# Kernel optimization log

Measured on AMD Instinct MI355X. Metric: run time of the kernel, lower is better.

Reference implementation:

```python
import jax, jax.numpy as jnp
import numpy as np

BN_EPS = 1e-5

def _square_distance(src, dst):
    # src [B,N,3], dst [B,S,3] -> [B,N,S]
    d = -2.0 * jnp.einsum('bnc,bsc->bns', src, dst)
    d = d + jnp.sum(src * src, -1)[:, :, None]
    d = d + jnp.sum(dst * dst, -1)[:, None, :]
    return d

def _conv_bn_relu(x, w, b, g, beta):
    # x [B,C,N]; 1x1 conv == channel GEMM, then training-mode batchnorm over (B,N)
    y = jnp.einsum('oc,bcn->bon', w, x) + b[None, :, None]
    mean = jnp.mean(y, axis=(0, 2), keepdims=True)
    var = jnp.mean((y - mean) ** 2, axis=(0, 2), keepdims=True)  # biased, as torch BN uses for normalization
    y = (y - mean) * jax.lax.rsqrt(var + BN_EPS)
    y = y * g[None, :, None] + beta[None, :, None]
    return jax.nn.relu(y)

def setup_inputs() -> dict:
    key = jax.random.key(0)
    ks = jax.random.split(key, 8)
    B, N, S, D1, D2 = 8, 8192, 2048, 128, 256
    C_in, C_mid, C_out = D1 + D2, 256, 256
    return {
        'xyz1': jax.random.normal(ks[0], (B, 3, N), jnp.float32),
        'xyz2': jax.random.normal(ks[1], (B, 3, S), jnp.float32),
        'points1': jax.random.normal(ks[2], (B, D1, N), jnp.float32),
        'points2': jax.random.normal(ks[3], (B, D2, S), jnp.float32),
        'w1': jax.random.normal(ks[4], (C_mid, C_in), jnp.float32) * (1.0 / np.sqrt(C_in)),
        'b1': jax.random.normal(ks[5], (C_mid,), jnp.float32) * 0.01,
        'g1': jnp.ones((C_mid,), jnp.float32),
        'beta1': jnp.zeros((C_mid,), jnp.float32),
        'w2': jax.random.normal(ks[6], (C_out, C_mid), jnp.float32) * (1.0 / np.sqrt(C_mid)),
        'b2': jax.random.normal(ks[7], (C_out,), jnp.float32) * 0.01,
        'g2': jnp.ones((C_out,), jnp.float32),
        'beta2': jnp.zeros((C_out,), jnp.float32),
    }

def reference(xyz1, xyz2, points1, points2, w1, b1, g1, beta1, w2, b2, g2, beta2):
    B = xyz1.shape[0]
    p1xyz = jnp.transpose(xyz1, (0, 2, 1))      # [B,N,3]
    p2xyz = jnp.transpose(xyz2, (0, 2, 1))      # [B,S,3]
    p2 = jnp.transpose(points2, (0, 2, 1))      # [B,S,D2]

    dists = _square_distance(p1xyz, p2xyz)      # [B,N,S]
    neg_d3, idx = jax.lax.top_k(-dists, 3)      # 3 smallest distances
    d3 = -neg_d3                                # [B,N,3]
    recip = 1.0 / (d3 + 1e-8)
    weight = recip / jnp.sum(recip, axis=2, keepdims=True)  # [B,N,3]

    gathered = jax.vmap(lambda p, i: p[i])(p2, idx)          # [B,N,3,D2]
    interp = jnp.sum(gathered * weight[..., None], axis=2)   # [B,N,D2]

    new_points = jnp.concatenate([jnp.transpose(points1, (0, 2, 1)), interp], axis=-1)
    x = jnp.transpose(new_points, (0, 2, 1))    # [B,D1+D2,N]
    x = _conv_bn_relu(x, w1, b1, g1, beta1)
    x = _conv_bn_relu(x, w2, b2, g2, beta2)
    return x
```

## Files before the change

### kernel.cpp

```cpp
#include <hip/hip_runtime.h>

#define B_    8
#define N_    8192
#define S_    2048
#define D1_   128
#define D2_   256
#define CIN_  384
#define CMID_ 256
#define COUT_ 256

typedef unsigned int  u32;
typedef unsigned short u16;
typedef __attribute__((ext_vector_type(8))) short short8;
typedef __attribute__((ext_vector_type(4))) float f32x4;

static __device__ __forceinline__ u32 uminu(u32 a, u32 b) { return a < b ? a : b; }
static __device__ __forceinline__ u32 umed3(u32 a, u32 b, u32 c) {
  u32 d;
  asm("v_med3_u32 %0, %1, %2, %3" : "=v"(d) : "v"(a), "v"(b), "v"(c));
  return d;
}
static __device__ __forceinline__ u16 f2bf(float f) {
  union { float f; u32 u; } v; v.f = f;
  u32 r = v.u + 0x7FFFu + ((v.u >> 16) & 1u);
  return (u16)(r >> 16);
}
static __device__ __forceinline__ float bflo(u32 u) { return __uint_as_float(u << 16); }
static __device__ __forceinline__ float bfhi(u32 u) { return __uint_as_float(u & 0xFFFF0000u); }
static __device__ __forceinline__ u32 cvtpk_bf16(float lo, float hi) {
  u32 d;
  asm("v_cvt_pk_bf16_f32 %0, %1, %2" : "=v"(d) : "v"(lo), "v"(hi));
  return d;
}

#define GLD16(g, l)                                                             \
  __builtin_amdgcn_global_load_lds((const __attribute__((address_space(1))) void*)(g), \
                                   (__attribute__((address_space(3))) void*)(l), 16, 0, 0)

#define WB(N)                                                                   \
  __builtin_amdgcn_sched_barrier(0);                                            \
  asm volatile("s_waitcnt vmcnt(" #N ")" ::: "memory");                         \
  __builtin_amdgcn_s_barrier();                                                 \
  __builtin_amdgcn_sched_barrier(0);

__global__ __launch_bounds__(256) void k_pre_all(const float* __restrict__ xyz2,
                                                 float4* __restrict__ pts4,
                                                 const float* __restrict__ w1,
                                                 const float* __restrict__ w2,
                                                 u16* __restrict__ w1b,
                                                 u16* __restrict__ w2b,
                                                 const float* __restrict__ p2,
                                                 float* __restrict__ p2T,
                                                 const float* __restrict__ p1,
                                                 u16* __restrict__ xT) {
  __shared__ float t[32][33];
  const int blk = blockIdx.x;
  const int cc = threadIdx.x & 31, rr = threadIdx.x >> 5;
  if (blk < 4096) {
    const int s0 = (blk & 63) * 32, d0 = ((blk >> 6) & 7) * 32, b = blk >> 9;
#pragma unroll
    for (int i = 0; i < 4; ++i) {
      int r = rr + i * 8;
      t[r][cc] = p2[((size_t)b * D2_ + d0 + r) * S_ + s0 + cc];
    }
    __syncthreads();
#pragma unroll
    for (int i = 0; i < 4; ++i) {
      int r = rr + i * 8;
      p2T[((size_t)b * S_ + s0 + r) * D2_ + d0 + cc] = t[cc][r];
    }
    return;
  }
  if (blk < 12288) {
    const int idx = blk - 4096;
    const int n0 = (idx & 255) * 32, c0 = ((idx >> 8) & 3) * 32, b = idx >> 10;
#pragma unroll
    for (int i = 0; i < 4; ++i) {
      int r = rr + i * 8;
      t[r][cc] = p1[((size_t)b * D1_ + c0 + r) * N_ + n0 + cc];
    }
    __syncthreads();
#pragma unroll
    for (int i = 0; i < 4; ++i) {
      int r = rr + i * 8;
      xT[((size_t)b * N_ + n0 + r) * CIN_ + c0 + cc] = f2bf(t[cc][r]);
    }
    return;
  }
  const int i = (blk - 12288) * 256 + threadIdx.x;
  if (i < B_ * S_) {
    const int b = i >> 11, s = i & (S_ - 1);
    const float* xb = xyz2 + (size_t)b * 3 * S_;
    float x = xb[s], y = xb[S_ + s], z = xb[2 * S_ + s];
    pts4[b * S_ + s] = make_float4(-2.f * x, -2.f * y, -2.f * z, x * x + y * y + z * z);
    return;
  }
  const int j = i - B_ * S_;
  if (j < CMID_ * CIN_) { w1b[j] = f2bf(w1[j]); return; }
  const int h = j - CMID_ * CIN_;
  if (h < COUT_ * CMID_) w2b[h] = f2bf(w2[h]);
}

__global__ __launch_bounds__(256) void k_nnref(const float* __restrict__ xyz1,
                                               const float4* __restrict__ pts4,
                                               int4* __restrict__ idx4,
                                               float4* __restrict__ w4) {
  __shared__ uint4 sk[4][64];
  const int b = blockIdx.y, t = threadIdx.x;
  const int nl = t & 63, chunk = t >> 6;
  const int n = blockIdx.x * 64 + nl;
  const float* pb = xyz1 + (size_t)b * 3 * N_;
  {
    const float px = pb[n], py = pb[N_ + n], pz = pb[2 * N_ + n];
    const float pn = px * px + py * py + pz * pz;
    const float4* __restrict__ P = pts4 + b * S_ + chunk * 512;
    u32 m0 = ~0u, m1 = ~0u, m2 = ~0u;
#pragma unroll 8
    for (int s = 0; s < 512; ++s) {
      float4 q = P[s];
      float d = fmaf(px, q.x, fmaf(py, q.y, fmaf(pz, q.z, pn + q.w)));
      d = fmaxf(d, 0.f);
      u32 k = (__float_as_uint(d) & 0xFFFFFE00u) | (u32)s;
      u32 m2n = umed3(m1, m2, k);
      m1 = umed3(m0, m1, k);
      m0 = uminu(m0, k);
      m2 = m2n;
    }
    uint4 v; v.x = m0; v.y = m1; v.z = m2; v.w = m2;
    sk[chunk][nl] = v;
  }
  __syncthreads();
  if (t < 64) {
    const double px = (double)pb[n], py = (double)pb[N_ + n], pz = (double)pb[2 * N_ + n];
    const double pn = px * px + py * py + pz * pz;
    double bd0 = 1e300, bd1 = 1e300, bd2 = 1e300;
    int bi0 = 1 << 30, bi1 = 1 << 30, bi2 = 1 << 30;
#pragma unroll
    for (int c = 0; c < 4; ++c) {
      uint4 kk = sk[c][t];
      u32 arr[3] = {kk.x, kk.y, kk.z};
#pragma unroll
      for (int j = 0; j < 3; ++j) {
        int s = c * 512 + (int)(arr[j] & 511u);
        float4 q = pts4[b * S_ + s];
        double x = (double)(q.x * -0.5f), y = (double)(q.y * -0.5f), z = (double)(q.z * -0.5f);
        double dot = px * x + py * y + pz * z;
        double d = -2.0 * dot + (pn + (x * x + y * y + z * z));
        if (d < bd2 || (d == bd2 && s < bi2)) {
          if (d < bd1 || (d == bd1 && s < bi1)) {
            bd2 = bd1; bi2 = bi1;
            if (d < bd0 || (d == bd0 && s < bi0)) { bd1 = bd0; bi1 = bi0; bd0 = d; bi0 = s; }
            else                                  { bd1 = d;  bi1 = s; }
          } else { bd2 = d; bi2 = s; }
        }
      }
    }
    float f0 = (float)bd0, f1 = (float)bd1, f2 = (float)bd2;
    float r0 = 1.f / (f0 + 1e-8f), r1 = 1.f / (f1 + 1e-8f), r2 = 1.f / (f2 + 1e-8f);
    float rs = r0 + r1 + r2;
    w4[(size_t)b * N_ + n]   = make_float4(r0 / rs, r1 / rs, r2 / rs, 0.f);
    idx4[(size_t)b * N_ + n] = make_int4(bi0, bi1, bi2, 0);
  }
}

__global__ __launch_bounds__(256) void k_gather_pack(const float* __restrict__ p2T,
                                                     const int4* __restrict__ idx4,
                                                     const float4* __restrict__ w4,
                                                     u16* __restrict__ xT) {
  const int b = blockIdx.y;
  const int wv = threadIdx.x >> 6, lane = threadIdx.x & 63;
  const int nbase = blockIdx.x * 16 + wv * 4;
  int4   id[4];
  float4 w[4];
#pragma unroll
  for (int i = 0; i < 4; ++i) {
    id[i] = idx4[(size_t)b * N_ + nbase + i];
    w[i]  = w4[(size_t)b * N_ + nbase + i];
  }
#pragma unroll
  for (int i = 0; i < 4; ++i) {
    const int n = nbase + i;
    const float4* r0 = (const float4*)(p2T + ((size_t)b * S_ + id[i].x) * D2_) + lane;
    const float4* r1 = (const float4*)(p2T + ((size_t)b * S_ + id[i].y) * D2_) + lane;
    const float4* r2 = (const float4*)(p2T + ((size_t)b * S_ + id[i].z) * D2_) + lane;
    float4 a = *r0, bb = *r1, cq = *r2;
    ushort4 pk;
    pk.x = f2bf(a.x * w[i].x + bb.x * w[i].y + cq.x * w[i].z);
    pk.y = f2bf(a.y * w[i].x + bb.y * w[i].y + cq.y * w[i].z);
    pk.z = f2bf(a.z * w[i].x + bb.z * w[i].y + cq.z * w[i].z);
    pk.w = f2bf(a.w * w[i].x + bb.w * w[i].y + cq.w * w[i].z);
    *(ushort4*)(xT + ((size_t)b * N_ + n) * CIN_ + D1_ + lane * 4) = pk;
  }
}

__global__ __launch_bounds__(64) void k_bnstat(const float* __restrict__ ps,
                                               const float* __restrict__ pq,
                                               const float* __restrict__ g,
                                               const float* __restrict__ beta,
                                               float* __restrict__ scale,
                                               float* __restrict__ shift) {
  const int o = blockIdx.x, l = threadIdx.x;
  float s = 0.f, q = 0.f;
#pragma unroll
  for (int i = 0; i < 8; ++i) {
    s += ps[(size_t)(i * 64 + l) * 256 + o];
    q += pq[(size_t)(i * 64 + l) * 256 + o];
  }
#pragma unroll
  for (int m = 1; m <= 32; m <<= 1) { s += __shfl_xor(s, m); q += __shfl_xor(q, m); }
  if (l == 0) {
    const float inv = 1.0f / (float)(B_ * N_);
    float mean = s * inv;
    float var = q * inv - mean * mean;
    float sc = g[o] / sqrtf(var + 1e-5f);
    scale[o] = sc;
    shift[o] = beta[o] - mean * sc;
  }
}

__global__ __launch_bounds__(512) void k_gemm1(const u16* __restrict__ Wb,
                                               const float* __restrict__ bias,
                                               const u16* __restrict__ xT,
                                               u16* __restrict__ y1T,
                                               float* __restrict__ psum,
                                               float* __restrict__ pssq) {
  __shared__ u16 As[3][8192];
  __shared__ u16 Bs[3][4096];
  __shared__ float s_sum[256], s_ssq[256];
  const int b = blockIdx.z, bn0 = blockIdx.x * 128;
  const int tid = threadIdx.x, w = tid >> 6, l = tid & 63;
  const int wm = w & 3, wn = w >> 2;
  const int lr = l >> 2, lc = l & 3;
  const int fm = l & 15, fq = l >> 4;
  const int clog = (lc ^ ((lr >> 1) & 3)) * 8;
  const int swz8 = (fq ^ ((fm >> 1) & 3)) * 8;
  f32x4 acc[4][4];
#pragma unroll
  for (int i = 0; i < 4; ++i)
#pragma unroll
    for (int j = 0; j < 4; ++j) acc[i][j] = (f32x4){0.f, 0.f, 0.f, 0.f};

  const int NK = CIN_ / 32;

#define STAGE1(kk, buf)                                                         \
  {                                                                             \
    const int k0_ = (kk) * 32;                                                  \
    _Pragma("unroll") for (int j_ = 0; j_ < 2; ++j_) {                          \
      int seg_ = w * 2 + j_, row_ = seg_ * 16 + lr;                             \
      GLD16(Wb + (size_t)row_ * CIN_ + k0_ + clog, &As[buf][seg_ * 512]);       \
    }                                                                           \
    int brow_ = w * 16 + lr;                                                    \
    GLD16(xT + ((size_t)b * N_ + bn0 + brow_) * CIN_ + k0_ + clog,              \
          &Bs[buf][w * 512]);                                                   \
  }

  STAGE1(0, 0);
  STAGE1(1, 1);
  int cur = 0;
  for (int kk = 0; kk < NK; ++kk) {
    if (kk + 1 < NK) { WB(3) } else { WB(0) }
    if (kk + 2 < NK) {
      int bt = cur + 2; if (bt >= 3) bt -= 3;
      STAGE1(kk + 2, bt);
    }
    short8 af[4], bfr[4];
#pragma unroll
    for (int f = 0; f < 4; ++f) {
      af[f]  = *(const short8*)&As[cur][(wm * 64 + f * 16 + fm) * 32 + swz8];
      bfr[f] = *(const short8*)&Bs[cur][(wn * 64 + f * 16 + fm) * 32 + swz8];
    }
#pragma unroll
    for (int i = 0; i < 4; ++i)
#pragma unroll
      for (int j = 0; j < 4; ++j)
        acc[i][j] = __builtin_amdgcn_mfma_f32_16x16x32_bf16(af[i], bfr[j], acc[i][j], 0, 0, 0);
    ++cur; if (cur == 3) cur = 0;
  }
#undef STAGE1

  if (tid < 256) { s_sum[tid] = 0.f; s_ssq[tid] = 0.f; }
  __syncthreads();
  u16* tb = y1T + ((size_t)b * 64 + (bn0 >> 7)) * 32768;
#pragma unroll
  for (int i = 0; i < 4; ++i) {
    int ob = wm * 64 + i * 16 + fq * 4;
    float4 b4 = *(const float4*)(bias + ob);
    float sv0 = 0, sv1 = 0, sv2 = 0, sv3 = 0, qv0 = 0, qv1 = 0, qv2 = 0, qv3 = 0;
#pragma unroll
    for (int j = 0; j < 4; ++j) {
      int nl = wn * 64 + j * 16 + fm;
      ushort4 pk;
      pk.x = f2bf(acc[i][j][0] + b4.x);
      pk.y = f2bf(acc[i][j][1] + b4.y);
      pk.z = f2bf(acc[i][j][2] + b4.z);
      pk.w = f2bf(acc[i][j][3] + b4.w);
      *(ushort4*)(tb + (size_t)(ob >> 5) * 4096 + nl * 32 + (ob & 31)) = pk;
      float v0 = bflo(pk.x), v1 = bflo(pk.y), v2 = bflo(pk.z), v3 = bflo(pk.w);
      sv0 += v0; sv1 += v1; sv2 += v2; sv3 += v3;
      qv0 = fmaf(v0, v0, qv0); qv1 = fmaf(v1, v1, qv1);
      qv2 = fmaf(v2, v2, qv2); qv3 = fmaf(v3, v3, qv3);
    }
#pragma unroll
    for (int m = 1; m <= 8; m <<= 1) {
      sv0 += __shfl_xor(sv0, m); sv1 += __shfl_xor(sv1, m);
      sv2 += __shfl_xor(sv2, m); sv3 += __shfl_xor(sv3, m);
      qv0 += __shfl_xor(qv0, m); qv1 += __shfl_xor(qv1, m);
      qv2 += __shfl_xor(qv2, m); qv3 += __shfl_xor(qv3, m);
    }
    if (fm == 0) {
      atomicAdd(&s_sum[ob + 0], sv0); atomicAdd(&s_sum[ob + 1], sv1);
      atomicAdd(&s_sum[ob + 2], sv2); atomicAdd(&s_sum[ob + 3], sv3);
      atomicAdd(&s_ssq[ob + 0], qv0); atomicAdd(&s_ssq[ob + 1], qv1);
      atomicAdd(&s_ssq[ob + 2], qv2); atomicAdd(&s_ssq[ob + 3], qv3);
    }
  }
  __syncthreads();
  if (tid < 256) {
    const int blk = blockIdx.x + 64 * blockIdx.z;
    psum[(size_t)blk * 256 + tid] = s_sum[tid];
    pssq[(size_t)blk * 256 + tid] = s_ssq[tid];
  }
}

__global__ __launch_bounds__(512) void k_gemm2(const u16* __restrict__ Wb2,
                                               const float* __restrict__ b2,
                                               const u16* __restrict__ y1T,
                                               const float* __restrict__ scale,
                                               const float* __restrict__ shift,
                                               u16* __restrict__ y2T,
                                               float* __restrict__ psum,
                                               float* __restrict__ pssq) {
  __shared__ u16 As[3][8192];
  __shared__ u16 Bs[3][4096];
  __shared__ float s_sum[256], s_ssq[256];
  __shared__ float s_sc[CMID_], s_sh[CMID_];
  const int b = blockIdx.z, bn0 = blockIdx.x * 128;
  const int tid = threadIdx.x, w = tid >> 6, l = tid & 63;
  const int wm = w & 3, wn = w >> 2;
  const int lr = l >> 2, lc = l & 3;
  const int fm = l & 15, fq = l >> 4;
  const int clog = (lc ^ ((lr >> 1) & 3)) * 8;
  const int swz8 = (fq ^ ((fm >> 1) & 3)) * 8;
  if (tid < 256) {
    s_sc[tid] = scale[tid];
    s_sh[tid] = shift[tid];
  }
  f32x4 acc[4][4];
#pragma unroll
  for (int i = 0; i < 4; ++i)
#pragma unroll
    for (int j = 0; j < 4; ++j) acc[i][j] = (f32x4){0.f, 0.f, 0.f, 0.f};

  const u16* tb = y1T + ((size_t)b * 64 + (bn0 >> 7)) * 32768;
  const int NK = CMID_ / 32;

#define STAGE2(kk, buf)                                                         \
  {                                                                             \
    const int k0_ = (kk) * 32;                                                  \
    _Pragma("unroll") for (int j_ = 0; j_ < 2; ++j_) {                          \
      int seg_ = w * 2 + j_, row_ = seg_ * 16 + lr;                             \
      GLD16(Wb2 + (size_t)row_ * CMID_ + k0_ + clog, &As[buf][seg_ * 512]);     \
    }                                                                           \
    int brow_ = w * 16 + lr;                                                    \
    GLD16(tb + (size_t)(kk) * 4096 + brow_ * 32 + clog, &Bs[buf][w * 512]);     \
  }

  STAGE2(0, 0);
  STAGE2(1, 1);
  int cur = 0;
  for (int kk = 0; kk < NK; ++kk) {
    if (kk + 1 < NK) { WB(3) } else { WB(0) }
    if (kk + 2 < NK) {
      int bt = cur + 2; if (bt >= 3) bt -= 3;
      STAGE2(kk + 2, bt);
    }
    const int kb = kk * 32 + fq * 8;
    float4 s0 = *(const float4*)&s_sc[kb], s1 = *(const float4*)&s_sc[kb + 4];
    float4 h0 = *(const float4*)&s_sh[kb], h1 = *(const float4*)&s_sh[kb + 4];
    short8 af[4], bfr[4];
#pragma unroll
    for (int f = 0; f < 4; ++f) {
      af[f] = *(const short8*)&As[cur][(wm * 64 + f * 16 + fm) * 32 + swz8];
      uint4 r = *(const uint4*)&Bs[cur][(wn * 64 + f * 16 + fm) * 32 + swz8];
      float v0 = fmaxf(fmaf(bflo(r.x), s0.x, h0.x), 0.f);
      float v1 = fmaxf(fmaf(bfhi(r.x), s0.y, h0.y), 0.f);
      float v2 = fmaxf(fmaf(bflo(r.y), s0.z, h0.z), 0.f);
      float v3 = fmaxf(fmaf(bfhi(r.y), s0.w, h0.w), 0.f);
      float v4 = fmaxf(fmaf(bflo(r.z), s1.x, h1.x), 0.f);
      float v5 = fmaxf(fmaf(bfhi(r.z), s1.y, h1.y), 0.f);
      float v6 = fmaxf(fmaf(bflo(r.w), s1.z, h1.z), 0.f);
      float v7 = fmaxf(fmaf(bfhi(r.w), s1.w, h1.w), 0.f);
      union { u32 u[4]; short8 s; } cv;
      cv.u[0] = cvtpk_bf16(v0, v1); cv.u[1] = cvtpk_bf16(v2, v3);
      cv.u[2] = cvtpk_bf16(v4, v5); cv.u[3] = cvtpk_bf16(v6, v7);
      bfr[f] = cv.s;
    }
#pragma unroll
    for (int i = 0; i < 4; ++i)
#pragma unroll
      for (int j = 0; j < 4; ++j)
        acc[i][j] = __builtin_amdgcn_mfma_f32_16x16x32_bf16(af[i], bfr[j], acc[i][j], 0, 0, 0);
    ++cur; if (cur == 3) cur = 0;
  }
#undef STAGE2

  if (tid < 256) { s_sum[tid] = 0.f; s_ssq[tid] = 0.f; }
  __syncthreads();
  u16* tb2 = y2T + ((size_t)b * 64 + (bn0 >> 7)) * 32768;
#pragma unroll
  for (int i = 0; i < 4; ++i) {
    int ob = wm * 64 + i * 16 + fq * 4;
    float4 b4 = *(const float4*)(b2 + ob);
    float sv0 = 0, sv1 = 0, sv2 = 0, sv3 = 0, qv0 = 0, qv1 = 0, qv2 = 0, qv3 = 0;
#pragma unroll
    for (int j = 0; j < 4; ++j) {
      int nl = wn * 64 + j * 16 + fm;
      ushort4 pk;
      pk.x = f2bf(acc[i][j][0] + b4.x);
      pk.y = f2bf(acc[i][j][1] + b4.y);
      pk.z = f2bf(acc[i][j][2] + b4.z);
      pk.w = f2bf(acc[i][j][3] + b4.w);
      *(ushort4*)(tb2 + (size_t)(ob >> 5) * 4096 + nl * 32 + (ob & 31)) = pk;
      float v0 = bflo(pk.x), v1 = bflo(pk.y), v2 = bflo(pk.z), v3 = bflo(pk.w);
      sv0 += v0; sv1 += v1; sv2 += v2; sv3 += v3;
      qv0 = fmaf(v0, v0, qv0); qv1 = fmaf(v1, v1, qv1);
      qv2 = fmaf(v2, v2, qv2); qv3 = fmaf(v3, v3, qv3);
    }
#pragma unroll
    for (int m = 1; m <= 8; m <<= 1) {
      sv0 += __shfl_xor(sv0, m); sv1 += __shfl_xor(sv1, m);
      sv2 += __shfl_xor(sv2, m); sv3 += __shfl_xor(sv3, m);
      qv0 += __shfl_xor(qv0, m); qv1 += __shfl_xor(qv1, m);
      qv2 += __shfl_xor(qv2, m); qv3 += __shfl_xor(qv3, m);
    }
    if (fm == 0) {
      atomicAdd(&s_sum[ob + 0], sv0); atomicAdd(&s_sum[ob + 1], sv1);
      atomicAdd(&s_sum[ob + 2], sv2); atomicAdd(&s_sum[ob + 3], sv3);
      atomicAdd(&s_ssq[ob + 0], qv0); atomicAdd(&s_ssq[ob + 1], qv1);
      atomicAdd(&s_ssq[ob + 2], qv2); atomicAdd(&s_ssq[ob + 3], qv3);
    }
  }
  __syncthreads();
  if (tid < 256) {
    const int blk = blockIdx.x + 64 * blockIdx.z;
    psum[(size_t)blk * 256 + tid] = s_sum[tid];
    pssq[(size_t)blk * 256 + tid] = s_ssq[tid];
  }
}

__global__ __launch_bounds__(256) void k_bn2t(const u16* __restrict__ y2T,
                                              const float* __restrict__ scale,
                                              const float* __restrict__ shift,
                                              float* __restrict__ out) {
  __shared__ float t[32][33];
  const int b = blockIdx.z, n0 = blockIdx.x * 32, o0 = blockIdx.y * 32;
  const int cc = threadIdx.x & 31, rr = threadIdx.x >> 5;
  const float sc = scale[o0 + cc], sh = shift[o0 + cc];
  const u16* tb = y2T + ((size_t)b * 64 + (n0 >> 7)) * 32768 +
                  (size_t)(o0 >> 5) * 4096 + (size_t)(n0 & 96) * 32;
#pragma unroll
  for (int i = 0; i < 4; ++i) {
    int r = rr + i * 8;
    float v = bflo((u32)tb[r * 32 + cc]);
    t[r][cc] = fmaxf(fmaf(v, sc, sh), 0.f);
  }
  __syncthreads();
#pragma unroll
  for (int i = 0; i < 4; ++i) {
    int r = rr + i * 8;
    out[((size_t)b * COUT_ + o0 + r) * N_ + n0 + cc] = t[cc][r];
  }
}

extern "C" void kernel_launch(void* const* d_in, const int* in_sizes, int n_in,
                              void* d_out, int out_size, void* d_ws, size_t ws_size,
                              hipStream_t stream) {
  const float* xyz1    = (const float*)d_in[0];
  const float* xyz2    = (const float*)d_in[1];
  const float* points1 = (const float*)d_in[2];
  const float* points2 = (const float*)d_in[3];
  const float* w1      = (const float*)d_in[4];
  const float* b1      = (const float*)d_in[5];
  const float* g1      = (const float*)d_in[6];
  const float* beta1   = (const float*)d_in[7];
  const float* w2      = (const float*)d_in[8];
  const float* b2      = (const float*)d_in[9];
  const float* g2      = (const float*)d_in[10];
  const float* beta2   = (const float*)d_in[11];
  float* out = (float*)d_out;

  char* ws = (char*)d_ws;
  size_t off = 0;
  u16*    xT    = (u16*)(ws + off);    off += (size_t)B_ * N_ * CIN_ * 2;
  u16*    y1T   = (u16*)(ws + off);    off += (size_t)B_ * N_ * CMID_ * 2;
  float*  p2T   = (float*)(ws + off);  off += (size_t)B_ * S_ * D2_ * 4;
  float4* pts4  = (float4*)(ws + off); off += (size_t)B_ * S_ * 16;
  int4*   idx4  = (int4*)(ws + off);   off += (size_t)B_ * N_ * 16;
  float4* w4    = (float4*)(ws + off); off += (size_t)B_ * N_ * 16;
  u16*    w1b   = (u16*)(ws + off);    off += (size_t)CMID_ * CIN_ * 2;
  u16*    w2b   = (u16*)(ws + off);    off += (size_t)COUT_ * CMID_ * 2;
  float*  stats = (float*)(ws + off);  off += 1024 * sizeof(float);
  float*  psx   = (float*)(ws + off);  off += (size_t)4 * 512 * 256 * 4;
  u16*    y2T   = xT;
  float* psum1 = psx;
  float* pssq1 = psum1 + 512 * 256;
  float* psum2 = pssq1 + 512 * 256;
  float* pssq2 = psum2 + 512 * 256;
  float* scale1 = stats,        * shift1 = stats + 256;
  float* scale2 = stats + 512,  * shift2 = stats + 768;

  k_pre_all    <<<dim3(12992), 256, 0, stream>>>(xyz2, pts4, w1, w2, w1b, w2b,
                                                 points2, p2T, points1, xT);
  k_nnref      <<<dim3(N_ / 64, B_), 256, 0, stream>>>(xyz1, pts4, idx4, w4);
  k_gather_pack<<<dim3(N_ / 16, B_), 256, 0, stream>>>(p2T, idx4, w4, xT);
  k_gemm1      <<<dim3(N_ / 128, 1, B_), 512, 0, stream>>>(w1b, b1, xT, y1T,
                                                           psum1, pssq1);
  k_bnstat     <<<dim3(CMID_), 64, 0, stream>>>(psum1, pssq1, g1, beta1, scale1, shift1);
  k_gemm2      <<<dim3(N_ / 128, 1, B_), 512, 0, stream>>>(w2b, b2, y1T,
                                                           scale1, shift1,
                                                           y2T, psum2, pssq2);
  k_bnstat     <<<dim3(COUT_), 64, 0, stream>>>(psum2, pssq2, g2, beta2, scale2, shift2);
  k_bn2t       <<<dim3(N_ / 32, COUT_ / 32, B_), 256, 0, stream>>>(y2T, scale2, shift2, out);
}
```

Baseline: 300.9 us.

## Merge nearest-neighbour search with transpose blocks into one kernel for overlap

```diff
diff --git a/kernel.cpp b/kernel.cpp
--- a/kernel.cpp
+++ b/kernel.cpp
@@ -43,51 +43,13 @@
   __builtin_amdgcn_s_barrier();                                                 \
   __builtin_amdgcn_sched_barrier(0);
 
-__global__ __launch_bounds__(256) void k_pre_all(const float* __restrict__ xyz2,
-                                                 float4* __restrict__ pts4,
-                                                 const float* __restrict__ w1,
-                                                 const float* __restrict__ w2,
-                                                 u16* __restrict__ w1b,
-                                                 u16* __restrict__ w2b,
-                                                 const float* __restrict__ p2,
-                                                 float* __restrict__ p2T,
-                                                 const float* __restrict__ p1,
-                                                 u16* __restrict__ xT) {
-  __shared__ float t[32][33];
-  const int blk = blockIdx.x;
-  const int cc = threadIdx.x & 31, rr = threadIdx.x >> 5;
-  if (blk < 4096) {
-    const int s0 = (blk & 63) * 32, d0 = ((blk >> 6) & 7) * 32, b = blk >> 9;
-#pragma unroll
-    for (int i = 0; i < 4; ++i) {
-      int r = rr + i * 8;
-      t[r][cc] = p2[((size_t)b * D2_ + d0 + r) * S_ + s0 + cc];
-    }
-    __syncthreads();
-#pragma unroll
-    for (int i = 0; i < 4; ++i) {
-      int r = rr + i * 8;
-      p2T[((size_t)b * S_ + s0 + r) * D2_ + d0 + cc] = t[cc][r];
-    }
-    return;
-  }
-  if (blk < 12288) {
-    const int idx = blk - 4096;
-    const int n0 = (idx & 255) * 32, c0 = ((idx >> 8) & 3) * 32, b = idx >> 10;
-#pragma unroll
-    for (int i = 0; i < 4; ++i) {
-      int r = rr + i * 8;
-      t[r][cc] = p1[((size_t)b * D1_ + c0 + r) * N_ + n0 + cc];
-    }
-    __syncthreads();
-#pragma unroll
-    for (int i = 0; i < 4; ++i) {
-      int r = rr + i * 8;
-      xT[((size_t)b * N_ + n0 + r) * CIN_ + c0 + cc] = f2bf(t[cc][r]);
-    }
-    return;
-  }
-  const int i = (blk - 12288) * 256 + threadIdx.x;
+__global__ __launch_bounds__(256) void k_pre0(const float* __restrict__ xyz2,
+                                              float4* __restrict__ pts4,
+                                              const float* __restrict__ w1,
+                                              const float* __restrict__ w2,
+                                              u16* __restrict__ w1b,
+                                              u16* __restrict__ w2b) {
+  const int i = blockIdx.x * 256 + threadIdx.x;
   if (i < B_ * S_) {
     const int b = i >> 11, s = i & (S_ - 1);
     const float* xb = xyz2 + (size_t)b * 3 * S_;
@@ -101,65 +63,108 @@
   if (h < COUT_ * CMID_) w2b[h] = f2bf(w2[h]);
 }
 
-__global__ __launch_bounds__(256) void k_nnref(const float* __restrict__ xyz1,
-                                               const float4* __restrict__ pts4,
-                                               int4* __restrict__ idx4,
-                                               float4* __restrict__ w4) {
-  __shared__ uint4 sk[4][64];
-  const int b = blockIdx.y, t = threadIdx.x;
-  const int nl = t & 63, chunk = t >> 6;
-  const int n = blockIdx.x * 64 + nl;
-  const float* pb = xyz1 + (size_t)b * 3 * N_;
-  {
-    const float px = pb[n], py = pb[N_ + n], pz = pb[2 * N_ + n];
-    const float pn = px * px + py * py + pz * pz;
-    const float4* __restrict__ P = pts4 + b * S_ + chunk * 512;
-    u32 m0 = ~0u, m1 = ~0u, m2 = ~0u;
+__global__ __launch_bounds__(256) void k_mega(const float* __restrict__ xyz1,
+                                              const float4* __restrict__ pts4,
+                                              int4* __restrict__ idx4,
+                                              float4* __restrict__ w4,
+                                              const float* __restrict__ p2,
+                                              float* __restrict__ p2T,
+                                              const float* __restrict__ p1,
+                                              u16* __restrict__ xT) {
+  __shared__ __align__(16) char smem[4352];
+  const int blk = blockIdx.x;
+  if (blk < 1024) {
+    uint4 (*sk)[64] = (uint4(*)[64])smem;
+    const int b = blk >> 7, t = threadIdx.x;
+    const int nl = t & 63;
+    const int chunk = __builtin_amdgcn_readfirstlane(t >> 6);
+    const int n = (blk & 127) * 64 + nl;
+    const float* pb = xyz1 + (size_t)b * 3 * N_;
+    {
+      const float px = pb[n], py = pb[N_ + n], pz = pb[2 * N_ + n];
+      const float pn = px * px + py * py + pz * pz;
+      const float4* __restrict__ P = pts4 + b * S_ + chunk * 512;
+      u32 m0 = ~0u, m1 = ~0u, m2 = ~0u;
 #pragma unroll 8
-    for (int s = 0; s < 512; ++s) {
-      float4 q = P[s];
-      float d = fmaf(px, q.x, fmaf(py, q.y, fmaf(pz, q.z, pn + q.w)));
-      d = fmaxf(d, 0.f);
-      u32 k = (__float_as_uint(d) & 0xFFFFFE00u) | (u32)s;
-      u32 m2n = umed3(m1, m2, k);
-      m1 = umed3(m0, m1, k);
-      m0 = uminu(m0, k);
-      m2 = m2n;
-    }
-    uint4 v; v.x = m0; v.y = m1; v.z = m2; v.w = m2;
-    sk[chunk][nl] = v;
-  }
-  __syncthreads();
-  if (t < 64) {
-    const double px = (double)pb[n], py = (double)pb[N_ + n], pz = (double)pb[2 * N_ + n];
-    const double pn = px * px + py * py + pz * pz;
-    double bd0 = 1e300, bd1 = 1e300, bd2 = 1e300;
-    int bi0 = 1 << 30, bi1 = 1 << 30, bi2 = 1 << 30;
-#pragma unroll
-    for (int c = 0; c < 4; ++c) {
-      uint4 kk = sk[c][t];
-      u32 arr[3] = {kk.x, kk.y, kk.z};
-#pragma unroll
-      for (int j = 0; j < 3; ++j) {
-        int s = c * 512 + (int)(arr[j] & 511u);
-        float4 q = pts4[b * S_ + s];
-        double x = (double)(q.x * -0.5f), y = (double)(q.y * -0.5f), z = (double)(q.z * -0.5f);
-        double dot = px * x + py * y + pz * z;
-        double d = -2.0 * dot + (pn + (x * x + y * y + z * z));
-        if (d < bd2 || (d == bd2 && s < bi2)) {
-          if (d < bd1 || (d == bd1 && s < bi1)) {
-            bd2 = bd1; bi2 = bi1;
-            if (d < bd0 || (d == bd0 && s < bi0)) { bd1 = bd0; bi1 = bi0; bd0 = d; bi0 = s; }
-            else                                  { bd1 = d;  bi1 = s; }
-          } else { bd2 = d; bi2 = s; }
+      for (int s = 0; s < 512; ++s) {
+        float4 q = P[s];
+        float d = fmaf(px, q.x, fmaf(py, q.y, fmaf(pz, q.z, pn + q.w)));
+        d = fmaxf(d, 0.f);
+        u32 k = (__float_as_uint(d) & 0xFFFFFE00u) | (u32)s;
+        u32 m2n = umed3(m1, m2, k);
+        m1 = umed3(m0, m1, k);
+        m0 = uminu(m0, k);
+        m2 = m2n;
+      }
+      uint4 v; v.x = m0; v.y = m1; v.z = m2; v.w = m2;
+      sk[chunk][nl] = v;
+    }
+    __syncthreads();
+    if (t < 64) {
+      const double px = (double)pb[n], py = (double)pb[N_ + n], pz = (double)pb[2 * N_ + n];
+      const double pn = px * px + py * py + pz * pz;
+      double bd0 = 1e300, bd1 = 1e300, bd2 = 1e300;
+      int bi0 = 1 << 30, bi1 = 1 << 30, bi2 = 1 << 30;
+#pragma unroll
+      for (int c = 0; c < 4; ++c) {
+        uint4 kk = sk[c][t];
+        u32 arr[3] = {kk.x, kk.y, kk.z};
+#pragma unroll
+        for (int j = 0; j < 3; ++j) {
+          int s = c * 512 + (int)(arr[j] & 511u);
+          float4 q = pts4[b * S_ + s];
+          double x = (double)(q.x * -0.5f), y = (double)(q.y * -0.5f), z = (double)(q.z * -0.5f);
+          double dot = px * x + py * y + pz * z;
+          double d = -2.0 * dot + (pn + (x * x + y * y + z * z));
+          if (d < bd2 || (d == bd2 && s < bi2)) {
+            if (d < bd1 || (d == bd1 && s < bi1)) {
+              bd2 = bd1; bi2 = bi1;
+              if (d < bd0 || (d == bd0 && s < bi0)) { bd1 = bd0; bi1 = bi0; bd0 = d; bi0 = s; }
+              else                                  { bd1 = d;  bi1 = s; }
+            } else { bd2 = d; bi2 = s; }
+          }
         }
       }
-    }
-    float f0 = (float)bd0, f1 = (float)bd1, f2 = (float)bd2;
-    float r0 = 1.f / (f0 + 1e-8f), r1 = 1.f / (f1 + 1e-8f), r2 = 1.f / (f2 + 1e-8f);
-    float rs = r0 + r1 + r2;
-    w4[(size_t)b * N_ + n]   = make_float4(r0 / rs, r1 / rs, r2 / rs, 0.f);
-    idx4[(size_t)b * N_ + n] = make_int4(bi0, bi1, bi2, 0);
+      float f0 = (float)bd0, f1 = (float)bd1, f2 = (float)bd2;
+      float r0 = 1.f / (f0 + 1e-8f), r1 = 1.f / (f1 + 1e-8f), r2 = 1.f / (f2 + 1e-8f);
+      float rs = r0 + r1 + r2;
+      w4[(size_t)b * N_ + n]   = make_float4(r0 / rs, r1 / rs, r2 / rs, 0.f);
+      idx4[(size_t)b * N_ + n] = make_int4(bi0, bi1, bi2, 0);
+    }
+    return;
+  }
+  float (*t2)[33] = (float(*)[33])smem;
+  const int cc = threadIdx.x & 31, rr = threadIdx.x >> 5;
+  if (blk < 5120) {
+    const int idx = blk - 1024;
+    const int s0 = (idx & 63) * 32, d0 = ((idx >> 6) & 7) * 32, b = idx >> 9;
+#pragma unroll
+    for (int i = 0; i < 4; ++i) {
+      int r = rr + i * 8;
+      t2[r][cc] = p2[((size_t)b * D2_ + d0 + r) * S_ + s0 + cc];
+    }
+    __syncthreads();
+#pragma unroll
+    for (int i = 0; i < 4; ++i) {
+      int r = rr + i * 8;
+      p2T[((size_t)b * S_ + s0 + r) * D2_ + d0 + cc] = t2[cc][r];
+    }
+    return;
+  }
+  {
+    const int idx = blk - 5120;
+    const int n0 = (idx & 255) * 32, c0 = ((idx >> 8) & 3) * 32, b = idx >> 10;
+#pragma unroll
+    for (int i = 0; i < 4; ++i) {
+      int r = rr + i * 8;
+      t2[r][cc] = p1[((size_t)b * D1_ + c0 + r) * N_ + n0 + cc];
+    }
+    __syncthreads();
+#pragma unroll
+    for (int i = 0; i < 4; ++i) {
+      int r = rr + i * 8;
+      xT[((size_t)b * N_ + n0 + r) * CIN_ + c0 + cc] = f2bf(t2[cc][r]);
+    }
   }
 }
 
@@ -509,9 +514,9 @@
   float* scale1 = stats,        * shift1 = stats + 256;
   float* scale2 = stats + 512,  * shift2 = stats + 768;
 
-  k_pre_all    <<<dim3(12992), 256, 0, stream>>>(xyz2, pts4, w1, w2, w1b, w2b,
+  k_pre0       <<<dim3(704), 256, 0, stream>>>(xyz2, pts4, w1, w2, w1b, w2b);
+  k_mega       <<<dim3(13312), 256, 0, stream>>>(xyz1, pts4, idx4, w4,
                                                  points2, p2T, points1, xT);
-  k_nnref      <<<dim3(N_ / 64, B_), 256, 0, stream>>>(xyz1, pts4, idx4, w4);
   k_gather_pack<<<dim3(N_ / 16, B_), 256, 0, stream>>>(p2T, idx4, w4, xT);
   k_gemm1      <<<dim3(N_ / 128, 1, B_), 512, 0, stream>>>(w1b, b1, xT, y1T,
                                                            psum1, pssq1);
```

Result: faster. 250.0 us (-16.9%).
